# Optimization experiments

Hardware: AMD Instinct MI355X
Metric: run time of the kernel (lower is better)

## Reference

```python
import jax, jax.numpy as jnp
import numpy as np

B = 16384
A_SCALE = 1.7159
S_SCALE = 2.0 / 3.0
CONNECTIONS = [[0,1,2],[1,2,3],[2,3,4],[3,4,5],[0,4,5],[0,1,5],
               [0,1,2,3],[1,2,3,4],[2,3,4,5],[0,3,4,5],[0,1,4,5],[0,1,2,5],
               [0,1,3,4],[1,2,4,5],[0,2,3,5],[0,1,2,3,4,5]]

def _c3_mask():
    m = np.zeros((16, 6, 1, 1), dtype=np.float32)
    for i, conns in enumerate(CONNECTIONS):
        m[i, conns, 0, 0] = 1.0
    return jnp.asarray(m)

C3_MASK = _c3_mask()

def tanh_act(x):
    return A_SCALE * jnp.tanh(S_SCALE * x)

def conv_valid(x, w):
    # x: (B, Cin, H, W), w: (Cout, Cin, k, k) -> (B, Cout, H-k+1, W-k+1)
    return jax.lax.conv_general_dilated(
        x, w, window_strides=(1, 1), padding='VALID',
        dimension_numbers=('NCHW', 'OIHW', 'NCHW'))

def pool_affine(x, w, b):
    # Faithful to the torch 'efficient' path: reshape(B,C,H/2,W/2,2,2).mean((4,5)).
    # (This is a row-major regrouping, NOT true 2x2 block pooling.)
    bsz, c, h, wd = x.shape
    y = x.reshape(bsz, c, h // 2, wd // 2, 2, 2).mean(axis=(4, 5))
    return w.reshape(1, c, 1, 1) * y + b.reshape(1, c, 1, 1)


def setup_inputs() -> dict:
    key = jax.random.key(0)
    ks = jax.random.split(key, 14)
    inp = {
        'x':     jax.random.normal(ks[0], (B, 1, 32, 32), jnp.float32),
        'w1':    jax.random.normal(ks[1], (6, 1, 5, 5), jnp.float32) * 0.2,
        'b1':    jnp.zeros((6,), jnp.float32),
        's2_w':  jnp.ones((6,), jnp.float32),
        's2_b':  jnp.zeros((6,), jnp.float32),
        'w3':    jax.random.normal(ks[2], (16, 6, 5, 5), jnp.float32) * 0.1,
        'b3':    jnp.zeros((16,), jnp.float32),
        's4_w':  jnp.ones((16,), jnp.float32),
        's4_b':  jnp.zeros((16,), jnp.float32),
        'w5':    jax.random.normal(ks[3], (120, 16, 5, 5), jnp.float32) * 0.05,
        'b5':    jnp.zeros((120,), jnp.float32),
        'f6_w':  jax.random.normal(ks[4], (84, 120), jnp.float32) * 0.09,
        'f6_b':  jnp.zeros((84,), jnp.float32),
        'rbf_w': jax.random.bernoulli(ks[5], 0.3, (10, 84)).astype(jnp.float32),
    }
    return inp


def reference(x, w1, b1, s2_w, s2_b, w3, b3, s4_w, s4_b, w5, b5, f6_w, f6_b, rbf_w):
    # C1: full conv 1->6, per-filter scalar bias
    h = conv_valid(x, w1) + b1.reshape(1, -1, 1, 1)          # (B,6,28,28)
    h = tanh_act(h)
    # S2: avg pool (efficient reshape semantics) + learnable affine
    h = tanh_act(pool_affine(h, s2_w, s2_b))                  # (B,6,14,14)
    # C3: sparsely-connected conv 6->16, implemented as masked full conv
    h = conv_valid(h, w3 * C3_MASK) + b3.reshape(1, -1, 1, 1)  # (B,16,10,10)
    h = tanh_act(h)
    # S4
    h = tanh_act(pool_affine(h, s4_w, s4_b))                  # (B,16,5,5)
    # C5: full conv 16->120 on 5x5 -> 1x1, squeeze to (B,120)
    h = conv_valid(h, w5) + b5.reshape(1, -1, 1, 1)
    h = tanh_act(h.reshape(h.shape[0], 120))                  # (B,120)
    # F6
    h = tanh_act(h @ f6_w.T + f6_b)                           # (B,84)
    # RBF: squared euclidean distance to each class bitmap
    diff = h[:, None, :] - rbf_w[None, :, :]                  # (B,10,84)
    return jnp.sum(diff * diff, axis=2)                       # (B,10)
```

## Files before the change

### kernel.cpp

```cpp
#include <hip/hip_runtime.h>
#include <cstdint>


typedef unsigned int u32;

union U32H2 { u32 u; _Float16 h[2]; };
__device__ __forceinline__ float f16lo(u32 v) { U32H2 a; a.u = v; return (float)a.h[0]; }
__device__ __forceinline__ float f16hi(u32 v) { U32H2 a; a.u = v; return (float)a.h[1]; }
__device__ __forceinline__ u32 packh2(float a, float b) {
    U32H2 x; x.h[0] = (_Float16)a; x.h[1] = (_Float16)b; return x.u;
}

typedef _Float16 h2v __attribute__((ext_vector_type(2)));
typedef _Float16 half8 __attribute__((ext_vector_type(8)));
typedef float f32x4 __attribute__((ext_vector_type(4)));
union U32V2 { u32 u; h2v v; };
union AB8 { u32 u[4]; half8 h; };

#if defined(__has_builtin)
#if __has_builtin(__builtin_amdgcn_fdot2)
#define HAVE_FDOT2 1
#endif
#endif

__device__ __forceinline__ float dot2(u32 a, u32 b, float c) {
    U32V2 x, y; x.u = a; y.u = b;
#ifdef HAVE_FDOT2
    return __builtin_amdgcn_fdot2(x.v, y.v, c, false);
#else
    return c + (float)x.v[0] * (float)y.v[0] + (float)x.v[1] * (float)y.v[1];
#endif
}

__device__ __forceinline__ float tact(float v) {
    float e = __expf(1.3333333333f * v);
    return 1.7159f * (1.0f - 2.0f * __builtin_amdgcn_rcpf(e + 1.0f));
}

__device__ const u32 C3_MB[16] = {
    0x07, 0x0E, 0x1C, 0x38, 0x31, 0x23, 0x0F, 0x1E,
    0x3C, 0x39, 0x33, 0x27, 0x1B, 0x36, 0x2D, 0x3F };

#define WPK_W1  0
#define WPK_W1S 96
#define WPK_W3A 192
#define WPK_W3S 1728
#define WPK_W5  3264
#define WPK_F6  32064
#define WPK_N   37104

__global__ __launch_bounds__(256) void k_wpack(
    const float* __restrict__ w1, const float* __restrict__ w3,
    const float* __restrict__ w5, const float* __restrict__ f6w,
    u32* __restrict__ wpk)
{
    const int idx = blockIdx.x * 256 + threadIdx.x;
    if (idx >= WPK_N) return;
    float a = 0.0f, b = 0.0f;
    if (idx < 192) {
        const int s = idx >= 96;
        const int t = idx - s * 96;
        if (t < 90) {
            int ch = t / 15, r = t % 15, ky = r / 3, q = r % 3;
            const float* w = w1 + ch * 25 + ky * 5;
            if (!s) { a = w[2 * q]; if (q < 2) b = w[2 * q + 1]; }
            else if (q == 0) { b = w[0]; }
            else { a = w[2 * q - 1]; b = w[2 * q]; }
        }
    } else if (idx < WPK_W5) {
        const int t2 = idx - WPK_W3A;
        const int s = t2 >= 1536;
        const int t = t2 - s * 1536;
        const int oc = t / 96, kp = t % 96;
        if (kp < 90) {
            int ic = kp / 15, rem = kp % 15, ky = rem / 3, q = rem % 3;
            if ((C3_MB[oc] >> ic) & 1) {
                const float* w = w3 + (oc * 6 + ic) * 25 + ky * 5;
                if (!s) { a = w[2 * q]; if (q < 2) b = w[2 * q + 1]; }
                else if (q == 0) { b = w[0]; }
                else { a = w[2 * q - 1]; b = w[2 * q]; }
            }
        }
    } else if (idx < WPK_F6) {
        int t = idx - WPK_W5;
        int c = t / 240, r = t % 240, g = r / 3, q = r % 3;
        a = w5[c * 400 + g * 5 + 2 * q];
        if (q < 2) b = w5[c * 400 + g * 5 + 2 * q + 1];
    } else {
        int t = idx - WPK_F6;
        int o = t / 60, i = t % 60;
        a = f6w[o * 120 + 2 * i];
        b = f6w[o * 120 + 2 * i + 1];
    }
    wpk[idx] = packh2(a, b);
}

__global__ __launch_bounds__(256) void k_tr(const float* __restrict__ x,
                                            u32* __restrict__ xp)
{
    __shared__ _Float16 lds[64 * 66];
    const int t = threadIdx.x;
    const int tb = blockIdx.x * 64;
    const int tp = blockIdx.y * 64;
    #pragma unroll
    for (int i = 0; i < 16; ++i) {
        int idx = i * 256 + t;
        int bl = idx >> 6, pl = idx & 63;
        lds[pl * 66 + bl] = (_Float16)x[(size_t)(tb + bl) * 1024 + tp + pl];
    }
    __syncthreads();
    #pragma unroll
    for (int j = 0; j < 8; ++j) {
        int idx = j * 256 + t;
        int pp = idx >> 6, bl = idx & 63;
        U32H2 u;
        u.h[0] = lds[(2 * pp) * 66 + bl];
        u.h[1] = lds[(2 * pp + 1) * 66 + bl];
        xp[(size_t)(blockIdx.y * 32 + pp) * 8192 + tb + bl] = u.u;
    }
}

__global__ __launch_bounds__(256) void k_c1s2(
    const u32* __restrict__ xp, const u32* __restrict__ wpk,
    const float* __restrict__ b1,
    const float* __restrict__ s2w, const float* __restrict__ s2b,
    u32* __restrict__ s2p, int ostr)
{
    const int sl = blockIdx.x * 256 + threadIdx.x;
    const int oy2 = blockIdx.y / 3;
    const int cp  = blockIdx.y % 3;
    const int y0 = 2 * oy2;
    const u32* xb = xp + sl;

    u32 wl[2][15], wls[2][15];
    #pragma unroll
    for (int a = 0; a < 2; ++a) {
        #pragma unroll
        for (int i = 0; i < 15; ++i) wl[a][i]  = wpk[WPK_W1  + (2 * cp + a) * 15 + i];
        #pragma unroll
        for (int i = 0; i < 15; ++i) wls[a][i] = wpk[WPK_W1S + (2 * cp + a) * 15 + i];
    }

    u32 cur[6][4];
    #pragma unroll
    for (int r = 0; r < 6; ++r)
        #pragma unroll
        for (int c = 0; c < 4; ++c)
            cur[r][c] = xb[(size_t)((y0 + r) * 16 + c) * 8192];

    float va[2][7], vb[2][7];

    #pragma unroll
    for (int qx = 0; qx < 7; ++qx) {
        float o[2][2][4];
        #pragma unroll
        for (int a = 0; a < 2; ++a) {
            const float bbv = b1[2 * cp + a];
            #pragma unroll
            for (int u = 0; u < 2; ++u)
                #pragma unroll
                for (int d = 0; d < 4; ++d) o[a][u][d] = bbv;
        }
        #pragma unroll
        for (int r = 0; r < 6; ++r) {
            #pragma unroll
            for (int u = 0; u < 2; ++u) {
                const int ky = r - u;
                if (ky < 0 || ky > 4) continue;
                #pragma unroll
                for (int a = 0; a < 2; ++a) {
                    const u32 w0 = wl[a][ky * 3 + 0];
                    const u32 w1 = wl[a][ky * 3 + 1];
                    const u32 w2 = wl[a][ky * 3 + 2];
                    const u32 v0 = wls[a][ky * 3 + 0];
                    const u32 v1 = wls[a][ky * 3 + 1];
                    const u32 v2 = wls[a][ky * 3 + 2];
                    o[a][u][0] = dot2(cur[r][0], w0, dot2(cur[r][1], w1, dot2(cur[r][2], w2, o[a][u][0])));
                    o[a][u][1] = dot2(cur[r][0], v0, dot2(cur[r][1], v1, dot2(cur[r][2], v2, o[a][u][1])));
                    o[a][u][2] = dot2(cur[r][1], w0, dot2(cur[r][2], w1, dot2(cur[r][3], w2, o[a][u][2])));
                    o[a][u][3] = dot2(cur[r][1], v0, dot2(cur[r][2], v1, dot2(cur[r][3], v2, o[a][u][3])));
                }
            }
        }
        #pragma unroll
        for (int a = 0; a < 2; ++a) {
            const int ch = 2 * cp + a;
            const float sw = s2w[ch], sb = s2b[ch];
            float m0 = 0.25f * (tact(o[a][0][0]) + tact(o[a][0][1]) + tact(o[a][0][2]) + tact(o[a][0][3]));
            float m1 = 0.25f * (tact(o[a][1][0]) + tact(o[a][1][1]) + tact(o[a][1][2]) + tact(o[a][1][3]));
            va[a][qx] = tact(sw * m0 + sb);
            vb[a][qx] = tact(sw * m1 + sb);
        }
        if (qx < 6) {
            #pragma unroll
            for (int r = 0; r < 6; ++r) {
                cur[r][0] = cur[r][2];
                cur[r][1] = cur[r][3];
                cur[r][2] = xb[(size_t)((y0 + r) * 16 + 2 * qx + 4) * 8192];
                cur[r][3] = xb[(size_t)((y0 + r) * 16 + 2 * qx + 5) * 8192];
            }
        }
    }
    #pragma unroll
    for (int a = 0; a < 2; ++a) {
        u32 o7[7];
        o7[0] = packh2(va[a][0], va[a][1]);
        o7[1] = packh2(va[a][2], va[a][3]);
        o7[2] = packh2(va[a][4], va[a][5]);
        o7[3] = packh2(va[a][6], vb[a][0]);
        o7[4] = packh2(vb[a][1], vb[a][2]);
        o7[5] = packh2(vb[a][3], vb[a][4]);
        o7[6] = packh2(vb[a][5], vb[a][6]);
        const int ch = 2 * cp + a;
        const int f0 = ch * 98 + oy2 * 7;
        const int fh0 = f0 >> 1;
        uint2* p2 = (uint2*)s2p;
        uint2 t;
        if ((oy2 & 1) == 0) {
            t.x = o7[0]; t.y = o7[1]; p2[(size_t)(fh0 + 0) * ostr + sl] = t;
            t.x = o7[2]; t.y = o7[3]; p2[(size_t)(fh0 + 1) * ostr + sl] = t;
            t.x = o7[4]; t.y = o7[5]; p2[(size_t)(fh0 + 2) * ostr + sl] = t;
            s2p[((size_t)(fh0 + 3) * ostr + sl) * 2] = o7[6];
        } else {
            s2p[((size_t)fh0 * ostr + sl) * 2 + 1] = o7[0];
            t.x = o7[1]; t.y = o7[2]; p2[(size_t)(fh0 + 1) * ostr + sl] = t;
            t.x = o7[3]; t.y = o7[4]; p2[(size_t)(fh0 + 2) * ostr + sl] = t;
            t.x = o7[5]; t.y = o7[6]; p2[(size_t)(fh0 + 3) * ostr + sl] = t;
        }
    }
}

__global__ __launch_bounds__(256) void k_c3s4m(
    const u32* __restrict__ s2p, const u32* __restrict__ wpk,
    const float* __restrict__ b3, const float* __restrict__ s4w,
    const float* __restrict__ s4b, u32* __restrict__ s4p, int nb)
{
    __shared__ u32 lds[252 * 65];
    const int t = threadIdx.x;
    const int y2 = blockIdx.y;
    const int base = blockIdx.x * 64;
    const uint2* s2c = (const uint2*)s2p;

    for (int i = 0; i < 32; ++i) {
        int idx = i * 256 + t;
        if (idx < 8064) {
            int ic = idx / 1344;
            int r = idx - ic * 1344;
            int cell = r >> 6, sLoc = r & 63;
            uint2 v = s2c[(size_t)(49 * ic + 7 * y2 + cell) * nb + base + sLoc];
            lds[(ic * 42 + 2 * cell) * 65 + sLoc]     = v.x;
            lds[(ic * 42 + 2 * cell + 1) * 65 + sLoc] = v.y;
        }
    }

    const int l = t & 63, w = t >> 6;
    const int g = l >> 4, col = l & 15;
    const int sLocal = w * 16 + col;
    const int ocA = col;

    AB8 wA[6], wS[6];
    #pragma unroll
    for (int s = 0; s < 6; ++s)
        #pragma unroll
        for (int m = 0; m < 4; ++m) {
            int kp = 16 * s + 4 * g + m;
            wA[s].u[m] = wpk[WPK_W3A + ocA * 96 + kp];
            wS[s].u[m] = wpk[WPK_W3S + ocA * 96 + kp];
        }

    int vbase[6][4];
    u32 zmask[4];
    #pragma unroll
    for (int s = 0; s < 6; ++s)
        #pragma unroll
        for (int m = 0; m < 4; ++m) {
            int kp = 16 * s + 4 * g + m;
            int ic = kp / 15;
            int rem = kp - ic * 15;
            int kr = rem / 3;
            int pr = rem - kr * 3;
            int c = ic * 42 + kr * 7 + pr;
            if (kp >= 90) c = 240;
            vbase[s][m] = c * 65 + sLocal;
            if (s == 5) zmask[m] = (kp < 90) ? 0xFFFFFFFFu : 0u;
        }

    float b3v[4], swv[4], sbv[4];
    #pragma unroll
    for (int r = 0; r < 4; ++r) {
        b3v[r] = b3[4 * g + r];
        swv[r] = s4w[4 * g + r];
        sbv[r] = s4b[4 * g + r];
    }

    __syncthreads();

    float pool[4][5];
    #pragma unroll
    for (int r = 0; r < 4; ++r)
        #pragma unroll
        for (int x2 = 0; x2 < 5; ++x2) pool[r][x2] = 0.0f;

    #pragma unroll
    for (int q = 0; q < 5; ++q) {
        f32x4 a00 = {0.f, 0.f, 0.f, 0.f};
        f32x4 a01 = {0.f, 0.f, 0.f, 0.f};
        f32x4 a10 = {0.f, 0.f, 0.f, 0.f};
        f32x4 a11 = {0.f, 0.f, 0.f, 0.f};
        #pragma unroll
        for (int s = 0; s < 6; ++s) {
            AB8 b0, b1;
            #pragma unroll
            for (int m = 0; m < 4; ++m) {
                u32 x0 = lds[vbase[s][m] + q * 65];
                u32 x1 = lds[vbase[s][m] + (q + 7) * 65];
                if (s == 5) { x0 &= zmask[m]; x1 &= zmask[m]; }
                b0.u[m] = x0; b1.u[m] = x1;
            }
            a00 = __builtin_amdgcn_mfma_f32_16x16x32_f16(wA[s].h, b0.h, a00, 0, 0, 0);
            a01 = __builtin_amdgcn_mfma_f32_16x16x32_f16(wS[s].h, b0.h, a01, 0, 0, 0);
            a10 = __builtin_amdgcn_mfma_f32_16x16x32_f16(wA[s].h, b1.h, a10, 0, 0, 0);
            a11 = __builtin_amdgcn_mfma_f32_16x16x32_f16(wS[s].h, b1.h, a11, 0, 0, 0);
        }
        #pragma unroll
        for (int r = 0; r < 4; ++r) {
            pool[r][(2 * q) >> 2]      += tact(a00[r] + b3v[r]);
            pool[r][(2 * q + 1) >> 2]  += tact(a01[r] + b3v[r]);
            pool[r][(10 + 2 * q) >> 2] += tact(a10[r] + b3v[r]);
            pool[r][(11 + 2 * q) >> 2] += tact(a11[r] + b3v[r]);
        }
    }

    const int sG = base + sLocal;
    #pragma unroll
    for (int r = 0; r < 4; ++r) {
        float so[5];
        #pragma unroll
        for (int x2 = 0; x2 < 5; ++x2)
            so[x2] = tact(0.25f * pool[r][x2] * swv[r] + sbv[r]);
        const int ocr = 4 * g + r;
        const size_t gf = (size_t)(ocr * 5 + y2) * 3;
        s4p[(gf + 0) * nb + sG] = packh2(so[0], so[1]);
        s4p[(gf + 1) * nb + sG] = packh2(so[2], so[3]);
        s4p[(gf + 2) * nb + sG] = packh2(so[4], 0.0f);
    }
}

__global__ __launch_bounds__(256) void k_c5(
    const u32* __restrict__ s4p, const u32* __restrict__ wpk,
    const float* __restrict__ b5, u32* __restrict__ h5p, int nb)
{
    const int sl = blockIdx.x * 256 + threadIdx.x;
    const int chg = blockIdx.y;
    const u32* wp = wpk + WPK_W5 + chg * 10 * 240;
    float acc[10];
    #pragma unroll
    for (int c = 0; c < 10; ++c) acc[c] = b5[chg * 10 + c];
    #pragma unroll 4
    for (int i = 0; i < 240; ++i) {
        const u32 v = s4p[(size_t)i * nb + sl];
        #pragma unroll
        for (int c = 0; c < 10; ++c)
            acc[c] = dot2(v, wp[c * 240 + i], acc[c]);
    }
    #pragma unroll
    for (int j = 0; j < 5; ++j)
        h5p[(size_t)(chg * 5 + j) * nb + sl] =
            packh2(tact(acc[2 * j]), tact(acc[2 * j + 1]));
}

__global__ __launch_bounds__(256) void k_f6(
    const u32* __restrict__ h5p, const u32* __restrict__ wpk,
    const float* __restrict__ f6b, u32* __restrict__ h6p, int nb)
{
    const int sl = blockIdx.x * 256 + threadIdx.x;
    const int og = blockIdx.y;
    const u32* wp = wpk + WPK_F6 + og * 14 * 60;
    float acc[14];
    #pragma unroll
    for (int o = 0; o < 14; ++o) acc[o] = f6b[og * 14 + o];
    #pragma unroll 4
    for (int i = 0; i < 60; ++i) {
        const u32 v = h5p[(size_t)i * nb + sl];
        #pragma unroll
        for (int o = 0; o < 14; ++o)
            acc[o] = dot2(v, wp[o * 60 + i], acc[o]);
    }
    #pragma unroll
    for (int j = 0; j < 7; ++j)
        h6p[(size_t)(og * 7 + j) * nb + sl] =
            packh2(tact(acc[2 * j]), tact(acc[2 * j + 1]));
}

__global__ __launch_bounds__(256) void k_rbf(
    const u32* __restrict__ h6p, const float* __restrict__ rbf,
    float* __restrict__ out, int nb)
{
    const int sl = blockIdx.x * 256 + threadIdx.x;
    const int gy = blockIdx.y;
    float hv[84];
    #pragma unroll
    for (int i = 0; i < 42; ++i) {
        const u32 v = h6p[(size_t)i * nb + sl];
        hv[2 * i]     = f16lo(v);
        hv[2 * i + 1] = f16hi(v);
    }
    #pragma unroll
    for (int a = 0; a < 2; ++a) {
        const int c = 2 * gy + a;
        float acc = 0.0f;
        #pragma unroll 4
        for (int i = 0; i < 84; ++i) {
            float d = hv[i] - rbf[c * 84 + i];
            acc += d * d;
        }
        out[(size_t)sl * 10 + c] = acc;
    }
}

extern "C" void kernel_launch(void* const* d_in, const int* in_sizes, int n_in,
                              void* d_out, int out_size, void* d_ws, size_t ws_size,
                              hipStream_t stream)
{
    const float* x    = (const float*)d_in[0];
    const float* w1   = (const float*)d_in[1];
    const float* b1   = (const float*)d_in[2];
    const float* s2w  = (const float*)d_in[3];
    const float* s2b  = (const float*)d_in[4];
    const float* w3   = (const float*)d_in[5];
    const float* b3   = (const float*)d_in[6];
    const float* s4w  = (const float*)d_in[7];
    const float* s4b  = (const float*)d_in[8];
    const float* w5   = (const float*)d_in[9];
    const float* b5   = (const float*)d_in[10];
    const float* f6w  = (const float*)d_in[11];
    const float* f6b  = (const float*)d_in[12];
    const float* rbfw = (const float*)d_in[13];
    float* out = (float*)d_out;
    char* ws = (char*)d_ws;

    u32* WPK = (u32*)((char*)d_out +
                      (((size_t)out_size - (size_t)(WPK_N * 4)) & ~(size_t)7));
    k_wpack<<<dim3((WPK_N + 255) / 256), 256, 0, stream>>>(w1, w3, w5, f6w, WPK);

    if (ws_size >= 55312384) {
        u32* S2P = (u32*)(ws);
        u32* XP  = (u32*)(ws + 38535168);
        u32* S4P = (u32*)(ws + 38535168);
        u32* H5P = (u32*)(ws);
        u32* H6P = (u32*)(ws + 4194304);
        for (int c = 0; c < 2; ++c) {
            k_tr  <<<dim3(128, 16), 256, 0, stream>>>(x + (size_t)c * 8192 * 1024, XP);
            k_c1s2<<<dim3(32, 42), 256, 0, stream>>>(XP, WPK, b1, s2w, s2b,
                                                     S2P + (size_t)c * 16384, 16384);
        }
        k_c3s4m<<<dim3(256, 5), 256, 0, stream>>>(S2P, WPK, b3, s4w, s4b, S4P, 16384);
        k_c5  <<<dim3(64, 12), 256, 0, stream>>>(S4P, WPK, b5, H5P, 16384);
        k_f6  <<<dim3(64, 6), 256, 0, stream>>>(H5P, WPK, f6b, H6P, 16384);
        k_rbf <<<dim3(64, 5), 256, 0, stream>>>(H6P, rbfw, out, 16384);
    } else {
        u32* XP  = (u32*)(ws);
        u32* S2P = (u32*)(ws + 16777216);
        u32* S4P = (u32*)(ws);
        u32* H5P = (u32*)(ws + 7864320);
        u32* H6P = (u32*)(ws + 9830400);
        for (int c = 0; c < 2; ++c) {
            k_tr  <<<dim3(128, 16), 256, 0, stream>>>(x + (size_t)c * 8192 * 1024, XP);
            k_c1s2<<<dim3(32, 42), 256, 0, stream>>>(XP, WPK, b1, s2w, s2b, S2P, 8192);
            k_c3s4m<<<dim3(128, 5), 256, 0, stream>>>(S2P, WPK, b3, s4w, s4b, S4P, 8192);
            k_c5  <<<dim3(32, 12), 256, 0, stream>>>(S4P, WPK, b5, H5P, 8192);
            k_f6  <<<dim3(32, 6), 256, 0, stream>>>(H5P, WPK, f6b, H6P, 8192);
            k_rbf <<<dim3(32, 5), 256, 0, stream>>>(H6P, rbfw, out + (size_t)c * 8192 * 10, 8192);
        }
    }
}
```

Baseline: 315.6 us.

## Rewrite C1+S2 conv as MFMA f16 matmul with LDS-staged input tiles

Replaces the per-thread fdot2 scalar convolution for C1 (with fused S2 pooling) with a 16x16x32 f16 MFMA formulation. A block stages the six input rows it needs for 64 samples into LDS and uses packed weights as the A operand, so all six output channels come from one wave group per block instead of being split across channel-pair blocks. The intent is to move the C1 arithmetic onto matrix cores and reduce redundant global input loads. In exchange it adds LDS traffic, a zero-padded region and partially idle MFMA lanes (12 of 16 rows and 3 of 4 groups used).

```diff
diff --git a/kernel.cpp b/kernel.cpp
--- a/kernel.cpp
+++ b/kernel.cpp
@@ -120,112 +120,130 @@
     }
 }
 
-__global__ __launch_bounds__(256) void k_c1s2(
+__global__ __launch_bounds__(256) void k_c1s2m(
     const u32* __restrict__ xp, const u32* __restrict__ wpk,
     const float* __restrict__ b1,
     const float* __restrict__ s2w, const float* __restrict__ s2b,
-    u32* __restrict__ s2p, int ostr)
-{
-    const int sl = blockIdx.x * 256 + threadIdx.x;
-    const int oy2 = blockIdx.y / 3;
-    const int cp  = blockIdx.y % 3;
+    u32* __restrict__ s2p, int nxp, int ostr)
+{
+    __shared__ u32 lds[126 * 65];
+    const int t = threadIdx.x;
+    const int oy2 = blockIdx.y;
+    const int base = blockIdx.x * 64;
     const int y0 = 2 * oy2;
-    const u32* xb = xp + sl;
-
-    u32 wl[2][15], wls[2][15];
-    #pragma unroll
-    for (int a = 0; a < 2; ++a) {
-        #pragma unroll
-        for (int i = 0; i < 15; ++i) wl[a][i]  = wpk[WPK_W1  + (2 * cp + a) * 15 + i];
-        #pragma unroll
-        for (int i = 0; i < 15; ++i) wls[a][i] = wpk[WPK_W1S + (2 * cp + a) * 15 + i];
-    }
-
-    u32 cur[6][4];
-    #pragma unroll
-    for (int r = 0; r < 6; ++r)
-        #pragma unroll
-        for (int c = 0; c < 4; ++c)
-            cur[r][c] = xb[(size_t)((y0 + r) * 16 + c) * 8192];
+
+    for (int i = t; i < 30 * 65; i += 256) lds[96 * 65 + i] = 0;
+    {
+        const uint2* xp2 = (const uint2*)xp;
+        const int nxp2 = nxp >> 1;
+        #pragma unroll
+        for (int i = 0; i < 12; ++i) {
+            int idx = i * 256 + t;
+            int cell = idx >> 5, sp = idx & 31;
+            uint2 v = xp2[(size_t)(y0 * 16 + cell) * nxp2 + (base >> 1) + sp];
+            lds[cell * 65 + 2 * sp]     = v.x;
+            lds[cell * 65 + 2 * sp + 1] = v.y;
+        }
+    }
+
+    const int l = t & 63, w = t >> 6;
+    const int g = l >> 4, col = l & 15;
+    const int sLocal = w * 16 + col;
+    const int rho = col;
+    const int ocw = rho >> 1, parw = rho & 1;
+
+    AB8 wA;
+    #pragma unroll
+    for (int m = 0; m < 4; ++m) {
+        int kp = 4 * g + m;
+        u32 v = 0;
+        if (rho < 12 && kp < 15)
+            v = wpk[(parw ? WPK_W1S : WPK_W1) + ocw * 15 + kp];
+        wA.u[m] = v;
+    }
+
+    int voff[4];
+    #pragma unroll
+    for (int m = 0; m < 4; ++m) {
+        int kp = 4 * g + m;
+        int c = (kp < 15) ? ((kp / 3) * 16 + kp % 3) : 96;
+        voff[m] = c * 65 + sLocal;
+    }
+
+    const int oc0 = 2 * g;
+    float b1v0 = 0.f, b1v1 = 0.f, sw0 = 0.f, sb0 = 0.f, sw1 = 0.f, sb1 = 0.f;
+    if (g < 3) {
+        b1v0 = b1[oc0];     b1v1 = b1[oc0 + 1];
+        sw0  = s2w[oc0];    sb0  = s2b[oc0];
+        sw1  = s2w[oc0 + 1]; sb1 = s2b[oc0 + 1];
+    }
+
+    __syncthreads();
 
     float va[2][7], vb[2][7];
 
     #pragma unroll
-    for (int qx = 0; qx < 7; ++qx) {
-        float o[2][2][4];
+    for (int q = 0; q < 7; ++q) {
+        f32x4 a00 = {0.f,0.f,0.f,0.f};
+        f32x4 a01 = {0.f,0.f,0.f,0.f};
+        f32x4 a10 = {0.f,0.f,0.f,0.f};
+        f32x4 a11 = {0.f,0.f,0.f,0.f};
+        AB8 b;
+        #pragma unroll
+        for (int m = 0; m < 4; ++m) b.u[m] = lds[voff[m] + (2 * q) * 65];
+        a00 = __builtin_amdgcn_mfma_f32_16x16x32_f16(wA.h, b.h, a00, 0, 0, 0);
+        #pragma unroll
+        for (int m = 0; m < 4; ++m) b.u[m] = lds[voff[m] + (2 * q + 1) * 65];
+        a01 = __builtin_amdgcn_mfma_f32_16x16x32_f16(wA.h, b.h, a01, 0, 0, 0);
+        #pragma unroll
+        for (int m = 0; m < 4; ++m) b.u[m] = lds[voff[m] + (16 + 2 * q) * 65];
+        a10 = __builtin_amdgcn_mfma_f32_16x16x32_f16(wA.h, b.h, a10, 0, 0, 0);
+        #pragma unroll
+        for (int m = 0; m < 4; ++m) b.u[m] = lds[voff[m] + (17 + 2 * q) * 65];
+        a11 = __builtin_amdgcn_mfma_f32_16x16x32_f16(wA.h, b.h, a11, 0, 0, 0);
+
+        float m00 = 0.25f * (tact(a00[0] + b1v0) + tact(a00[1] + b1v0) +
+                             tact(a01[0] + b1v0) + tact(a01[1] + b1v0));
+        float m01 = 0.25f * (tact(a00[2] + b1v1) + tact(a00[3] + b1v1) +
+                             tact(a01[2] + b1v1) + tact(a01[3] + b1v1));
+        float m10 = 0.25f * (tact(a10[0] + b1v0) + tact(a10[1] + b1v0) +
+                             tact(a11[0] + b1v0) + tact(a11[1] + b1v0));
+        float m11 = 0.25f * (tact(a10[2] + b1v1) + tact(a10[3] + b1v1) +
+                             tact(a11[2] + b1v1) + tact(a11[3] + b1v1));
+        va[0][q] = tact(sw0 * m00 + sb0);
+        vb[0][q] = tact(sw0 * m10 + sb0);
+        va[1][q] = tact(sw1 * m01 + sb1);
+        vb[1][q] = tact(sw1 * m11 + sb1);
+    }
+
+    if (g < 3) {
+        const int sl = base + sLocal;
         #pragma unroll
         for (int a = 0; a < 2; ++a) {
-            const float bbv = b1[2 * cp + a];
-            #pragma unroll
-            for (int u = 0; u < 2; ++u)
-                #pragma unroll
-                for (int d = 0; d < 4; ++d) o[a][u][d] = bbv;
-        }
-        #pragma unroll
-        for (int r = 0; r < 6; ++r) {
-            #pragma unroll
-            for (int u = 0; u < 2; ++u) {
-                const int ky = r - u;
-                if (ky < 0 || ky > 4) continue;
-                #pragma unroll
-                for (int a = 0; a < 2; ++a) {
-                    const u32 w0 = wl[a][ky * 3 + 0];
-                    const u32 w1 = wl[a][ky * 3 + 1];
-                    const u32 w2 = wl[a][ky * 3 + 2];
-                    const u32 v0 = wls[a][ky * 3 + 0];
-                    const u32 v1 = wls[a][ky * 3 + 1];
-                    const u32 v2 = wls[a][ky * 3 + 2];
-                    o[a][u][0] = dot2(cur[r][0], w0, dot2(cur[r][1], w1, dot2(cur[r][2], w2, o[a][u][0])));
-                    o[a][u][1] = dot2(cur[r][0], v0, dot2(cur[r][1], v1, dot2(cur[r][2], v2, o[a][u][1])));
-                    o[a][u][2] = dot2(cur[r][1], w0, dot2(cur[r][2], w1, dot2(cur[r][3], w2, o[a][u][2])));
-                    o[a][u][3] = dot2(cur[r][1], v0, dot2(cur[r][2], v1, dot2(cur[r][3], v2, o[a][u][3])));
-                }
+            u32 o7[7];
+            o7[0] = packh2(va[a][0], va[a][1]);
+            o7[1] = packh2(va[a][2], va[a][3]);
+            o7[2] = packh2(va[a][4], va[a][5]);
+            o7[3] = packh2(va[a][6], vb[a][0]);
+            o7[4] = packh2(vb[a][1], vb[a][2]);
+            o7[5] = packh2(vb[a][3], vb[a][4]);
+            o7[6] = packh2(vb[a][5], vb[a][6]);
+            const int ch = oc0 + a;
+            const int f0 = ch * 98 + oy2 * 7;
+            const int fh0 = f0 >> 1;
+            uint2* p2 = (uint2*)s2p;
+            uint2 tt;
+            if ((oy2 & 1) == 0) {
+                tt.x = o7[0]; tt.y = o7[1]; p2[(size_t)(fh0 + 0) * ostr + sl] = tt;
+                tt.x = o7[2]; tt.y = o7[3]; p2[(size_t)(fh0 + 1) * ostr + sl] = tt;
+                tt.x = o7[4]; tt.y = o7[5]; p2[(size_t)(fh0 + 2) * ostr + sl] = tt;
+                s2p[((size_t)(fh0 + 3) * ostr + sl) * 2] = o7[6];
+            } else {
+                s2p[((size_t)fh0 * ostr + sl) * 2 + 1] = o7[0];
+                tt.x = o7[1]; tt.y = o7[2]; p2[(size_t)(fh0 + 1) * ostr + sl] = tt;
+                tt.x = o7[3]; tt.y = o7[4]; p2[(size_t)(fh0 + 2) * ostr + sl] = tt;
+                tt.x = o7[5]; tt.y = o7[6]; p2[(size_t)(fh0 + 3) * ostr + sl] = tt;
             }
-        }
-        #pragma unroll
-        for (int a = 0; a < 2; ++a) {
-            const int ch = 2 * cp + a;
-            const float sw = s2w[ch], sb = s2b[ch];
-            float m0 = 0.25f * (tact(o[a][0][0]) + tact(o[a][0][1]) + tact(o[a][0][2]) + tact(o[a][0][3]));
-            float m1 = 0.25f * (tact(o[a][1][0]) + tact(o[a][1][1]) + tact(o[a][1][2]) + tact(o[a][1][3]));
-            va[a][qx] = tact(sw * m0 + sb);
-            vb[a][qx] = tact(sw * m1 + sb);
-        }
-        if (qx < 6) {
-            #pragma unroll
-            for (int r = 0; r < 6; ++r) {
-                cur[r][0] = cur[r][2];
-                cur[r][1] = cur[r][3];
-                cur[r][2] = xb[(size_t)((y0 + r) * 16 + 2 * qx + 4) * 8192];
-                cur[r][3] = xb[(size_t)((y0 + r) * 16 + 2 * qx + 5) * 8192];
-            }
-        }
-    }
-    #pragma unroll
-    for (int a = 0; a < 2; ++a) {
-        u32 o7[7];
-        o7[0] = packh2(va[a][0], va[a][1]);
-        o7[1] = packh2(va[a][2], va[a][3]);
-        o7[2] = packh2(va[a][4], va[a][5]);
-        o7[3] = packh2(va[a][6], vb[a][0]);
-        o7[4] = packh2(vb[a][1], vb[a][2]);
-        o7[5] = packh2(vb[a][3], vb[a][4]);
-        o7[6] = packh2(vb[a][5], vb[a][6]);
-        const int ch = 2 * cp + a;
-        const int f0 = ch * 98 + oy2 * 7;
-        const int fh0 = f0 >> 1;
-        uint2* p2 = (uint2*)s2p;
-        uint2 t;
-        if ((oy2 & 1) == 0) {
-            t.x = o7[0]; t.y = o7[1]; p2[(size_t)(fh0 + 0) * ostr + sl] = t;
-            t.x = o7[2]; t.y = o7[3]; p2[(size_t)(fh0 + 1) * ostr + sl] = t;
-            t.x = o7[4]; t.y = o7[5]; p2[(size_t)(fh0 + 2) * ostr + sl] = t;
-            s2p[((size_t)(fh0 + 3) * ostr + sl) * 2] = o7[6];
-        } else {
-            s2p[((size_t)fh0 * ostr + sl) * 2 + 1] = o7[0];
-            t.x = o7[1]; t.y = o7[2]; p2[(size_t)(fh0 + 1) * ostr + sl] = t;
-            t.x = o7[3]; t.y = o7[4]; p2[(size_t)(fh0 + 2) * ostr + sl] = t;
-            t.x = o7[5]; t.y = o7[6]; p2[(size_t)(fh0 + 3) * ostr + sl] = t;
         }
     }
 }
@@ -451,8 +469,9 @@
         u32* H6P = (u32*)(ws + 4194304);
         for (int c = 0; c < 2; ++c) {
             k_tr  <<<dim3(128, 16), 256, 0, stream>>>(x + (size_t)c * 8192 * 1024, XP);
-            k_c1s2<<<dim3(32, 42), 256, 0, stream>>>(XP, WPK, b1, s2w, s2b,
-                                                     S2P + (size_t)c * 16384, 16384);
+            k_c1s2m<<<dim3(128, 14), 256, 0, stream>>>(XP, WPK, b1, s2w, s2b,
+                                                       S2P + (size_t)c * 16384,
+                                                       8192, 16384);
         }
         k_c3s4m<<<dim3(256, 5), 256, 0, stream>>>(S2P, WPK, b3, s4w, s4b, S4P, 16384);
         k_c5  <<<dim3(64, 12), 256, 0, stream>>>(S4P, WPK, b5, H5P, 16384);
@@ -466,7 +485,8 @@
         u32* H6P = (u32*)(ws + 9830400);
         for (int c = 0; c < 2; ++c) {
             k_tr  <<<dim3(128, 16), 256, 0, stream>>>(x + (size_t)c * 8192 * 1024, XP);
-            k_c1s2<<<dim3(32, 42), 256, 0, stream>>>(XP, WPK, b1, s2w, s2b, S2P, 8192);
+            k_c1s2m<<<dim3(128, 14), 256, 0, stream>>>(XP, WPK, b1, s2w, s2b,
+                                                       S2P, 8192, 8192);
             k_c3s4m<<<dim3(128, 5), 256, 0, stream>>>(S2P, WPK, b3, s4w, s4b, S4P, 8192);
             k_c5  <<<dim3(32, 12), 256, 0, stream>>>(S4P, WPK, b5, H5P, 8192);
             k_f6  <<<dim3(32, 6), 256, 0, stream>>>(H5P, WPK, f6b, H6P, 8192);
```

After: 298.3 us. 5.5% less time.
